# Kernel tuning notes

Hardware: AMD Instinct MI355X
Metric: run time of the kernel (lower is better)

The kernel has to match this reference:

```python
import jax, jax.numpy as jnp
import numpy as np

D = 256  # rst_input_dim


def _gru_cell(x, h, W_ih, W_hh, b_ih, b_hh):
    # x, h: (..., D); W_*: (3D, D); PyTorch GRU gate order: r, z, n
    gi = x @ W_ih.T + b_ih          # (..., 3D)
    gh = h @ W_hh.T + b_hh
    i_r, i_z, i_n = jnp.split(gi, 3, axis=-1)
    h_r, h_z, h_n = jnp.split(gh, 3, axis=-1)
    r = jax.nn.sigmoid(i_r + h_r)
    z = jax.nn.sigmoid(i_z + h_z)
    n = jnp.tanh(i_n + r * h_n)
    return (1.0 - z) * n + z * h


def setup_inputs() -> dict:
    key = jax.random.key(0)
    ks = jax.random.split(key, 5)
    B, L = 32, 4096
    s = 1.0 / np.sqrt(D)
    return {
        "leaf_embeds": jax.random.normal(ks[0], (B, L, D), dtype=jnp.float32),
        "W_ih": jax.random.normal(ks[1], (3 * D, D), dtype=jnp.float32) * s,
        "W_hh": jax.random.normal(ks[2], (3 * D, D), dtype=jnp.float32) * s,
        "b_ih": jax.random.normal(ks[3], (3 * D,), dtype=jnp.float32) * s,
        "b_hh": jax.random.normal(ks[4], (3 * D,), dtype=jnp.float32) * s,
    }


def reference(leaf_embeds, W_ih, W_hh, b_ih, b_hh):
    # Post-order traversal of a perfect binary tree, batched level-by-level
    # (classic tree-RNN same-depth batching). Leaves: embed = EDU embedding,
    # hidden = zeros. Internal node: h0 = mean(h_left, h_right); run GRU over
    # the 2-step sequence [left_embed, right_embed]; out = mean of the two
    # GRU outputs; returned hidden = final GRU hidden.
    embeds = leaf_embeds                      # (B, N, D)
    hs = jnp.zeros_like(leaf_embeds)          # (B, N, D)
    n = embeds.shape[1]
    while n > 1:
        xL, xR = embeds[:, 0::2], embeds[:, 1::2]   # (B, n/2, D)
        hL, hR = hs[:, 0::2], hs[:, 1::2]
        h0 = 0.5 * (hL + hR)                         # mean of child hiddens
        h1 = _gru_cell(xL, h0, W_ih, W_hh, b_ih, b_hh)
        h2 = _gru_cell(xR, h1, W_ih, W_hh, b_ih, b_hh)
        embeds = 0.5 * (h1 + h2)                     # mean over seq outputs
        hs = h2
        n //= 2
    return embeds[:, 0]                              # (B, D): root embedding
```

## Files before the change

### kernel.cpp

```cpp
#include <hip/hip_runtime.h>
#include <hip/hip_bf16.h>
#include <stdint.h>

typedef _Float16 f16x8 __attribute__((ext_vector_type(8)));
typedef float    f32x4 __attribute__((ext_vector_type(4)));

#define GLDS16(gptr, lptr) \
  __builtin_amdgcn_global_load_lds((const __attribute__((address_space(1))) void*)(gptr), \
                                   (__attribute__((address_space(3))) void*)(lptr), 16, 0, 0)

__global__ __launch_bounds__(256) void prepack_weights(
    const float* __restrict__ Wih, const float* __restrict__ Whh,
    const float* __restrict__ bih, const float* __restrict__ bhh,
    _Float16* __restrict__ WP, float* __restrict__ BC)
{
    if (blockIdx.x == 2048) {
        int i = threadIdx.x;
        BC[i]       = bih[i] + bhh[i];
        BC[256 + i] = bih[256 + i] + bhh[256 + i];
        BC[512 + i] = bih[512 + i];
        BC[768 + i] = bhh[512 + i];
        return;
    }
    int idx = blockIdx.x * 256 + threadIdx.x;
    int j   = idx & 7;
    int nl  = (idx >> 3) & 63;
    int sub = (idx >> 9) & 7;
    int g   = (idx >> 12) & 3;
    int d0b = (idx >> 14) & 3;
    int c   = idx >> 16;
    int k = c * 64 + sub * 8 + j;
    int d = d0b * 64 + nl;
    float v = 0.f;
    if (g == 0)      v = (k < 256) ? Wih[d * 256 + k]         : Whh[d * 256 + (k - 256)];
    else if (g == 1) v = (k < 256) ? Wih[(256 + d) * 256 + k] : Whh[(256 + d) * 256 + (k - 256)];
    else if (g == 2) v = (k < 256) ? Wih[(512 + d) * 256 + k] : 0.f;
    else             v = (k >= 256) ? Whh[(512 + d) * 256 + (k - 256)] : 0.f;
    WP[idx] = (_Float16)v;
}

__global__ __launch_bounds__(256) void convert_split(
    const float* __restrict__ leaf, _Float16* __restrict__ XE, _Float16* __restrict__ XO)
{
    int t = blockIdx.x * 256 + threadIdx.x;
    size_t e = (size_t)t * 4;
    int row = (int)(e >> 8), col = (int)(e & 255);
    float4 v = *(const float4*)(leaf + e);
    _Float16* dst = ((row & 1) ? XO : XE) + ((size_t)(row >> 1) * 256 + col);
    union { _Float16 h[4]; uint64_t u; } p;
    p.h[0] = (_Float16)v.x; p.h[1] = (_Float16)v.y;
    p.h[2] = (_Float16)v.z; p.h[3] = (_Float16)v.w;
    *(uint64_t*)dst = p.u;
}

template<int MT, bool SWIZ>
__global__ __launch_bounds__(256, (MT == 8) ? 2 : 3) void gru_cell(
    const _Float16* __restrict__ Xsrc,
    const _Float16* __restrict__ Hsrc,
    const _Float16* __restrict__ WP,
    const float* __restrict__ BC,
    _Float16* __restrict__ Hout,
    _Float16* __restrict__ Ee, _Float16* __restrict__ Eo, _Float16* __restrict__ HP,
    int M)
{
    constexpr int AROW = MT * 16 * 8;
    constexpr int ASZ  = 8 * AROW;
    constexpr int BROW = 512;
    constexpr int BSZ  = 3 * 8 * BROW;
    __shared__ __align__(16) _Float16 Alds[2 * ASZ];
    __shared__ __align__(16) _Float16 Blds[2 * BSZ];

    const int tid  = threadIdx.x;
    int bm, d0b;
    if (SWIZ) {
        int xcd = blockIdx.x & 7, slot = blockIdx.x >> 3;
        d0b = slot & 3;
        bm  = (slot >> 2) * 8 + xcd;
    } else {
        bm = blockIdx.x >> 2; d0b = blockIdx.x & 3;
    }
    const int m0   = bm * (MT * 16);
    const int wave = tid >> 6, lane = tid & 63;
    const int quad = lane >> 4, lo = lane & 15;

    const bool has_h = (Hsrc != nullptr);
    const int nch = has_h ? 8 : 4;

    f32x4 acc[MT][4];
#pragma unroll
    for (int a = 0; a < MT; ++a)
#pragma unroll
        for (int b = 0; b < 4; ++b) acc[a][b] = (f32x4){0.f, 0.f, 0.f, 0.f};
    float hinv[MT][4];

    auto issueB = [&](int c) {
        const size_t cb = (size_t)(c * 4 + d0b) * 4;
        _Float16* dstb = Blds + (c & 1) * BSZ;
#pragma unroll
        for (int i = 0; i < 6; ++i) {
            int bi = wave * 6 + i;
            int slot = bi >> 3, sub = bi & 7;
            int g = (slot == 2) ? ((c < 4) ? 2 : 3) : slot;
            GLDS16(WP + ((cb + g) * 8 + sub) * 512 + lane * 8,
                   dstb + (slot * 8 + sub) * BROW);
        }
    };

    auto issueA = [&](int c) {
        const _Float16* base = (c < 4) ? Xsrc : Hsrc;
        const int coloff = (c & 3) * 64;
        _Float16* Ab = Alds + (c & 1) * ASZ;
        constexpr int IPS = MT / 4;
#pragma unroll
        for (int i = 0; i < MT / 2; ++i) {
            int ai = wave * (MT / 2) + i;
            int sub = ai / IPS, mh = ai % IPS;
            int row = m0 + mh * 64 + lane;
            if (MT == 4 && row >= M) row = M - 1;
            GLDS16(base + (size_t)row * 256 + coloff + sub * 8,
                   Ab + sub * AROW + mh * 64 * 8);
        }
    };

    issueB(0);
    issueA(0);

    for (int c = 0; c < nch; ++c) {
        __syncthreads();
        if (c + 1 < nch) {
            issueB(c + 1);
            issueA(c + 1);
        }

        const _Float16* Bb = Blds + (c & 1) * BSZ;
        const _Float16* Ab = Alds + (c & 1) * ASZ;
#pragma unroll
        for (int ks = 0; ks < 2; ++ks) {
            const int subb = ks * 4 + quad;
            const _Float16* brow = Bb + subb * BROW + (wave * 16 + lo) * 8;
            f16x8 b0 = *(const f16x8*)(brow);
            f16x8 b1 = *(const f16x8*)(brow + 8 * BROW);
            f16x8 b2 = *(const f16x8*)(brow + 16 * BROW);
            f16x8 af[MT];
#pragma unroll
            for (int mt = 0; mt < MT; ++mt)
                af[mt] = *(const f16x8*)(Ab + subb * AROW + (mt * 16 + lo) * 8);
#pragma unroll
            for (int mt = 0; mt < MT; ++mt)
                acc[mt][0] = __builtin_amdgcn_mfma_f32_16x16x32_f16(af[mt], b0, acc[mt][0], 0, 0, 0);
#pragma unroll
            for (int mt = 0; mt < MT; ++mt)
                acc[mt][1] = __builtin_amdgcn_mfma_f32_16x16x32_f16(af[mt], b1, acc[mt][1], 0, 0, 0);
            if (c < 4) {
#pragma unroll
                for (int mt = 0; mt < MT; ++mt)
                    acc[mt][2] = __builtin_amdgcn_mfma_f32_16x16x32_f16(af[mt], b2, acc[mt][2], 0, 0, 0);
            } else {
#pragma unroll
                for (int mt = 0; mt < MT; ++mt)
                    acc[mt][3] = __builtin_amdgcn_mfma_f32_16x16x32_f16(af[mt], b2, acc[mt][3], 0, 0, 0);
            }
        }

        if (has_h && c == 4 + d0b) {
            const _Float16* Ab2 = Alds + (c & 1) * ASZ;
            const int colw = wave * 16 + lo;
            const int sub = colw >> 3, j = colw & 7;
#pragma unroll
            for (int mt = 0; mt < MT; ++mt)
#pragma unroll
                for (int r = 0; r < 4; ++r)
                    hinv[mt][r] = (float)Ab2[sub * AROW + (mt * 16 + quad * 4 + r) * 8 + j];
        }
    }

    const int d = d0b * 64 + wave * 16 + lo;
    const float brz0 = BC[d];
    const float brz1 = BC[256 + d];
    const float bni  = BC[512 + d];
    const float bnh  = BC[768 + d];
#pragma unroll
    for (int mt = 0; mt < MT; ++mt) {
        const int mbase = m0 + mt * 16 + quad * 4;
        float hq[4], h1v[4];
#pragma unroll
        for (int r = 0; r < 4; ++r) {
            float hin = has_h ? hinv[mt][r] : 0.f;
            h1v[r] = hin;
            float rg = 1.f / (1.f + __expf(-(acc[mt][0][r] + brz0)));
            float zg = 1.f / (1.f + __expf(-(acc[mt][1][r] + brz1)));
            float ex = __expf(2.f * (acc[mt][2][r] + bni + rg * (acc[mt][3][r] + bnh)));
            float nv = 1.f - 2.f / (ex + 1.f);
            hq[r] = (1.f - zg) * nv + zg * hin;
        }
        if (Hout) {
#pragma unroll
            for (int r = 0; r < 4; ++r)
                if (MT == 8 || mbase + r < M)
                    Hout[(size_t)(mbase + r) * 256 + d] = (_Float16)hq[r];
        } else {
#pragma unroll
            for (int r = 0; r < 4; ++r) {
                int m = mbase + r;
                if (MT == 8 || m < M)
                    (((m & 1) ? Eo : Ee))[(size_t)(m >> 1) * 256 + d] =
                        (_Float16)(0.5f * (h1v[r] + hq[r]));
            }
            if (MT == 8 || mbase + 1 < M)
                HP[(size_t)(mbase >> 1) * 256 + d] = (_Float16)(0.5f * (hq[0] + hq[1]));
            if (MT == 8 || mbase + 3 < M)
                HP[(size_t)((mbase >> 1) + 1) * 256 + d] = (_Float16)(0.5f * (hq[2] + hq[3]));
        }
    }
}

__global__ __launch_bounds__(256) void final_out(
    const _Float16* __restrict__ XE, const _Float16* __restrict__ XO,
    float* __restrict__ out)
{
    int i = blockIdx.x * 256 + threadIdx.x;
    int j = i >> 8, col = i & 255;
    const _Float16* src = (j & 1) ? XO : XE;
    out[i] = (float)src[(size_t)(j >> 1) * 256 + col];
}

extern "C" void kernel_launch(void* const* d_in, const int* in_sizes, int n_in,
                              void* d_out, int out_size, void* d_ws, size_t ws_size,
                              hipStream_t stream) {
    const float* leaf = (const float*)d_in[0];
    const float* Wih  = (const float*)d_in[1];
    const float* Whh  = (const float*)d_in[2];
    const float* bih  = (const float*)d_in[3];
    const float* bhh  = (const float*)d_in[4];

    char* ws = (char*)d_ws;
    _Float16* WPp = (_Float16*)ws;
    _Float16* XAe = (_Float16*)(ws + (1ull  << 20));
    _Float16* XAo = (_Float16*)(ws + (33ull << 20));
    _Float16* XBe = (_Float16*)(ws + (65ull << 20));
    _Float16* XBo = (_Float16*)(ws + (81ull << 20));
    _Float16* H1  = (_Float16*)(ws + (97ull << 20));
    _Float16* HPb = (_Float16*)(ws + (129ull << 20));
    float*    BCp = (float*)(ws + (145ull << 20));

    prepack_weights<<<2049, 256, 0, stream>>>(Wih, Whh, bih, bhh, WPp, BCp);
    convert_split<<<32768, 256, 0, stream>>>(leaf, XAe, XAo);

    _Float16 *XeC = XAe, *XoC = XAo, *XeN = XBe, *XoN = XBo;
    const _Float16* hp = nullptr;
    int M = 65536;
    for (int lev = 0; lev < 12; ++lev) {
        if (M >= 8192) {
            int grid = (M / 128) * 4;
            gru_cell<8, true><<<grid, 256, 0, stream>>>(XeC, hp, WPp, BCp,
                                                        H1, nullptr, nullptr, nullptr, M);
            gru_cell<8, true><<<grid, 256, 0, stream>>>(XoC, H1, WPp, BCp,
                                                        nullptr, XeN, XoN, HPb, M);
        } else {
            int nbm = (M + 63) / 64;
            int grid = nbm * 4;
            if ((nbm & 7) == 0) {
                gru_cell<4, true><<<grid, 256, 0, stream>>>(XeC, hp, WPp, BCp,
                                                            H1, nullptr, nullptr, nullptr, M);
                gru_cell<4, true><<<grid, 256, 0, stream>>>(XoC, H1, WPp, BCp,
                                                            nullptr, XeN, XoN, HPb, M);
            } else {
                gru_cell<4, false><<<grid, 256, 0, stream>>>(XeC, hp, WPp, BCp,
                                                             H1, nullptr, nullptr, nullptr, M);
                gru_cell<4, false><<<grid, 256, 0, stream>>>(XoC, H1, WPp, BCp,
                                                             nullptr, XeN, XoN, HPb, M);
            }
        }
        hp = HPb;
        _Float16* t;
        t = XeC; XeC = XeN; XeN = t;
        t = XoC; XoC = XoN; XoN = t;
        M >>= 1;
    }
    final_out<<<32, 256, 0, stream>>>(XeC, XoC, (float*)d_out);
}
```

Before: 704.6 us.

## Store activations in 64-row tiled layout and stage epilogue writes through LDS

Activations (X, H, embeds, parent hiddens) switch from row-major to a tiled layout of 64-row by 8-column blocks, so each A-operand load becomes a contiguous 1KB chunk per wave. The GRU epilogue now writes results into LDS first and then emits coalesced 16-byte vector stores in the same tiled layout, replacing scattered 2-byte column stores. The conversion kernel and the final output kernel are updated to the new layout. Row-bound clamping for partial tiles is dropped, which assumes M is a multiple of the tile size at every level, including the small late levels.

```diff
diff --git a/kernel.cpp b/kernel.cpp
--- a/kernel.cpp
+++ b/kernel.cpp
@@ -8,6 +8,10 @@
 #define GLDS16(gptr, lptr) \
   __builtin_amdgcn_global_load_lds((const __attribute__((address_space(1))) void*)(gptr), \
                                    (__attribute__((address_space(3))) void*)(lptr), 16, 0, 0)
+
+__device__ __forceinline__ int tile_off(int rb, int c, int sub) {
+    return ((rb * 4 + c) * 8 + sub) * 512;
+}
 
 __global__ __launch_bounds__(256) void prepack_weights(
     const float* __restrict__ Wih, const float* __restrict__ Whh,
@@ -42,15 +46,18 @@
 __global__ __launch_bounds__(256) void convert_split(
     const float* __restrict__ leaf, _Float16* __restrict__ XE, _Float16* __restrict__ XO)
 {
-    int t = blockIdx.x * 256 + threadIdx.x;
-    size_t e = (size_t)t * 4;
-    int row = (int)(e >> 8), col = (int)(e & 255);
-    float4 v = *(const float4*)(leaf + e);
-    _Float16* dst = ((row & 1) ? XO : XE) + ((size_t)(row >> 1) * 256 + col);
-    union { _Float16 h[4]; uint64_t u; } p;
-    p.h[0] = (_Float16)v.x; p.h[1] = (_Float16)v.y;
-    p.h[2] = (_Float16)v.z; p.h[3] = (_Float16)v.w;
-    *(uint64_t*)dst = p.u;
+    int g = blockIdx.x * 256 + threadIdx.x;
+    int u = g & 31;
+    int row = g >> 5;
+    const float* src = leaf + (size_t)row * 256 + u * 8;
+    float4 a = *(const float4*)src;
+    float4 b = *(const float4*)(src + 4);
+    f16x8 p;
+    p[0] = (_Float16)a.x; p[1] = (_Float16)a.y; p[2] = (_Float16)a.z; p[3] = (_Float16)a.w;
+    p[4] = (_Float16)b.x; p[5] = (_Float16)b.y; p[6] = (_Float16)b.z; p[7] = (_Float16)b.w;
+    int ro = row >> 1;
+    _Float16* dst = (row & 1) ? XO : XE;
+    *(f16x8*)(dst + tile_off(ro >> 6, u >> 3, u & 7) + (ro & 63) * 8) = p;
 }
 
 template<int MT, bool SWIZ>
@@ -63,6 +70,7 @@
     _Float16* __restrict__ Ee, _Float16* __restrict__ Eo, _Float16* __restrict__ HP,
     int M)
 {
+    (void)M;
     constexpr int AROW = MT * 16 * 8;
     constexpr int ASZ  = 8 * AROW;
     constexpr int BROW = 512;
@@ -79,7 +87,6 @@
     } else {
         bm = blockIdx.x >> 2; d0b = blockIdx.x & 3;
     }
-    const int m0   = bm * (MT * 16);
     const int wave = tid >> 6, lane = tid & 63;
     const int quad = lane >> 4, lo = lane & 15;
 
@@ -108,17 +115,16 @@
 
     auto issueA = [&](int c) {
         const _Float16* base = (c < 4) ? Xsrc : Hsrc;
-        const int coloff = (c & 3) * 64;
+        const int cc = c & 3;
         _Float16* Ab = Alds + (c & 1) * ASZ;
-        constexpr int IPS = MT / 4;
-#pragma unroll
-        for (int i = 0; i < MT / 2; ++i) {
-            int ai = wave * (MT / 2) + i;
-            int sub = ai / IPS, mh = ai % IPS;
-            int row = m0 + mh * 64 + lane;
-            if (MT == 4 && row >= M) row = M - 1;
-            GLDS16(base + (size_t)row * 256 + coloff + sub * 8,
-                   Ab + sub * AROW + mh * 64 * 8);
+        constexpr int ND = MT / 2;
+#pragma unroll
+        for (int i = 0; i < ND; ++i) {
+            int ai = wave * ND + i;
+            int sub = (MT == 8) ? (ai >> 1) : ai;
+            int mh  = (MT == 8) ? (ai & 1) : 0;
+            GLDS16(base + tile_off(bm * (MT / 4) + mh, cc, sub) + lane * 8,
+                   Ab + sub * AROW + mh * 512);
         }
     };
 
@@ -174,42 +180,64 @@
         }
     }
 
-    const int d = d0b * 64 + wave * 16 + lo;
+    const int ld = wave * 16 + lo;
+    const int d  = d0b * 64 + ld;
     const float brz0 = BC[d];
     const float brz1 = BC[256 + d];
     const float bni  = BC[512 + d];
     const float bnh  = BC[768 + d];
+    constexpr int SROW = 72;
+    constexpr int PR   = MT * 8;
+    __syncthreads();
 #pragma unroll
     for (int mt = 0; mt < MT; ++mt) {
-        const int mbase = m0 + mt * 16 + quad * 4;
-        float hq[4], h1v[4];
+        const int lr0 = mt * 16 + quad * 4;
+        float hq[4];
 #pragma unroll
         for (int r = 0; r < 4; ++r) {
             float hin = has_h ? hinv[mt][r] : 0.f;
-            h1v[r] = hin;
             float rg = 1.f / (1.f + __expf(-(acc[mt][0][r] + brz0)));
             float zg = 1.f / (1.f + __expf(-(acc[mt][1][r] + brz1)));
             float ex = __expf(2.f * (acc[mt][2][r] + bni + rg * (acc[mt][3][r] + bnh)));
             float nv = 1.f - 2.f / (ex + 1.f);
             hq[r] = (1.f - zg) * nv + zg * hin;
-        }
-        if (Hout) {
-#pragma unroll
-            for (int r = 0; r < 4; ++r)
-                if (MT == 8 || mbase + r < M)
-                    Hout[(size_t)(mbase + r) * 256 + d] = (_Float16)hq[r];
-        } else {
-#pragma unroll
-            for (int r = 0; r < 4; ++r) {
-                int m = mbase + r;
-                if (MT == 8 || m < M)
-                    (((m & 1) ? Eo : Ee))[(size_t)(m >> 1) * 256 + d] =
-                        (_Float16)(0.5f * (h1v[r] + hq[r]));
+            int lr = lr0 + r;
+            if (Hout) {
+                Alds[lr * SROW + ld] = (_Float16)hq[r];
+            } else {
+                Alds[(((lr & 1) * PR) + (lr >> 1)) * SROW + ld] =
+                    (_Float16)(0.5f * (hin + hq[r]));
             }
-            if (MT == 8 || mbase + 1 < M)
-                HP[(size_t)(mbase >> 1) * 256 + d] = (_Float16)(0.5f * (hq[0] + hq[1]));
-            if (MT == 8 || mbase + 3 < M)
-                HP[(size_t)((mbase >> 1) + 1) * 256 + d] = (_Float16)(0.5f * (hq[2] + hq[3]));
+        }
+        if (!Hout) {
+            Alds[(2 * PR + (lr0 >> 1)) * SROW + ld]     = (_Float16)(0.5f * (hq[0] + hq[1]));
+            Alds[(2 * PR + (lr0 >> 1) + 1) * SROW + ld] = (_Float16)(0.5f * (hq[2] + hq[3]));
+        }
+    }
+    __syncthreads();
+
+    if (Hout) {
+        constexpr int NU = MT * 128;
+#pragma unroll
+        for (int i = 0; i < NU / 256; ++i) {
+            int uid = i * 256 + tid;
+            int r = uid & 63, sub = (uid >> 6) & 7, mh = uid >> 9;
+            f16x8 v = *(const f16x8*)&Alds[(mh * 64 + r) * SROW + sub * 8];
+            *(f16x8*)(Hout + tile_off(bm * (MT / 4) + mh, d0b, sub) + r * 8) = v;
+        }
+    } else {
+        constexpr int NU = 3 * PR * 8;
+        const int rbE  = (MT == 8) ? bm : (bm >> 1);
+        const int roff = (MT == 8) ? 0 : (bm & 1) * 32;
+#pragma unroll
+        for (int i = 0; i < NU / 256; ++i) {
+            int uid = i * 256 + tid;
+            int pr   = uid & (PR - 1);
+            int rest = uid / PR;
+            int sub = rest & 7, buf = rest >> 3;
+            f16x8 v = *(const f16x8*)&Alds[(buf * PR + pr) * SROW + sub * 8];
+            _Float16* dst = (buf == 0) ? Ee : (buf == 1) ? Eo : HP;
+            *(f16x8*)(dst + tile_off(rbE, d0b, sub) + (roff + pr) * 8) = v;
         }
     }
 }
@@ -221,7 +249,8 @@
     int i = blockIdx.x * 256 + threadIdx.x;
     int j = i >> 8, col = i & 255;
     const _Float16* src = (j & 1) ? XO : XE;
-    out[i] = (float)src[(size_t)(j >> 1) * 256 + col];
+    int r = j >> 1;
+    out[i] = (float)src[tile_off(0, col >> 6, (col >> 3) & 7) + r * 8 + (col & 7)];
 }
 
 extern "C" void kernel_launch(void* const* d_in, const int* in_sizes, int n_in,
@@ -244,7 +273,7 @@
     float*    BCp = (float*)(ws + (145ull << 20));
 
     prepack_weights<<<2049, 256, 0, stream>>>(Wih, Whh, bih, bhh, WPp, BCp);
-    convert_split<<<32768, 256, 0, stream>>>(leaf, XAe, XAo);
+    convert_split<<<16384, 256, 0, stream>>>(leaf, XAe, XAo);
 
     _Float16 *XeC = XAe, *XoC = XAo, *XeN = XBe, *XoN = XBo;
     const _Float16* hp = nullptr;
```

Result: faster. 673.4 us (-4.4%).
